# Performance work log

Measured on AMD Instinct MI355X. Metric: run time of the kernel, lower is better.

The kernel has to match this reference:

```python
import jax, jax.numpy as jnp
import numpy as np

B_SZ = 8
G = 2048
D_MODEL = 512
D_STATE = 128
D_CONV = 4
EXPAND = 2
HEADDIM = 64
D_INNER = EXPAND * D_MODEL          # 1024
NHEADS = D_INNER // HEADDIM         # 16
CONV_DIM = D_INNER + 2 * D_STATE    # 1280
D_IN_PROJ = 2 * D_INNER + 2 * D_STATE + NHEADS  # 2320
ID_DIM = 128
CHR_DIM = 64
N_CHR = 25
F_LOCUS = 32
PATH_DIM = 128
GENE_FEAT = ID_DIM + PATH_DIM + 2 * CHR_DIM  # 384
N_PERT = 10000
P_DIM = 128


def silu(x):
    return x * jax.nn.sigmoid(x)


def causal_dw_conv(x, w, b):
    # x: (B,L,C), w: (C,K), b: (C,)  causal depthwise conv (left pad K-1)
    K = w.shape[1]
    L = x.shape[1]
    xp = jnp.pad(x, ((0, 0), (K - 1, 0), (0, 0)))
    out = b[None, None, :]
    for k in range(K):
        out = out + xp[:, k:k + L, :] * w[:, k][None, None, :]
    return out


def mamba2(u, in_w, conv_w, conv_b, dt_bias, A_log, Dp, norm_w, out_w):
    # u: (B,L,d_model) -> (B,L,d_model); mamba_ssm Mamba2 defaults, ngroups=1
    Bb, L, _ = u.shape
    zxbcdt = u @ in_w.T                                   # (B,L,D_IN_PROJ)
    z = zxbcdt[..., :D_INNER]
    xBC = zxbcdt[..., D_INNER:D_INNER + CONV_DIM]
    dt = zxbcdt[..., D_INNER + CONV_DIM:]                 # (B,L,H)
    xBC = silu(causal_dw_conv(xBC, conv_w, conv_b))
    x = xBC[..., :D_INNER].reshape(Bb, L, NHEADS, HEADDIM)
    Bm = xBC[..., D_INNER:D_INNER + D_STATE]              # (B,L,N)
    Cm = xBC[..., D_INNER + D_STATE:]                     # (B,L,N)
    dt = jax.nn.softplus(dt + dt_bias)                    # (B,L,H)
    dA = jnp.exp(dt * (-jnp.exp(A_log)))                  # (B,L,H)

    def step(h, inp):
        dA_t, dt_t, B_t, C_t, x_t = inp
        h = dA_t[:, :, None, None] * h + jnp.einsum('bh,bn,bhp->bhpn', dt_t, B_t, x_t)
        y = jnp.einsum('bhpn,bn->bhp', h, C_t)
        return h, y

    h0 = jnp.zeros((Bb, NHEADS, HEADDIM, D_STATE), u.dtype)
    xs = (dA.transpose(1, 0, 2), dt.transpose(1, 0, 2),
          Bm.transpose(1, 0, 2), Cm.transpose(1, 0, 2), x.transpose(1, 0, 2, 3))
    _, ys = jax.lax.scan(step, h0, xs)                    # ys: (L,B,H,P)
    y = ys.transpose(1, 0, 2, 3) + Dp[None, None, :, None] * x
    y = y.reshape(Bb, L, D_INNER)
    # gated RMSNorm (norm_before_gate=False): norm(y * silu(z))
    y = y * silu(z)
    y = y * jax.lax.rsqrt(jnp.mean(y * y, axis=-1, keepdims=True) + 1e-5) * norm_w
    return y @ out_w.T


def setup_inputs() -> dict:
    key = jax.random.key(0)
    ks = iter(jax.random.split(key, 48))

    def nrm(shape, scale):
        return jax.random.normal(next(ks), shape, jnp.float32) * scale

    inp = {}
    inp['perturbation_idx'] = jax.random.randint(next(ks), (B_SZ,), 0, N_PERT)
    inp['chr_idx'] = jax.random.randint(next(ks), (G,), 0, N_CHR)
    inp['locus_fourier'] = nrm((G, 2 * F_LOCUS), 1.0)
    inp['pathway_features'] = nrm((G, PATH_DIM), 1.0)
    inp['pert_emb'] = nrm((N_PERT, P_DIM), 0.02)
    inp['gene_id_emb'] = nrm((G, ID_DIM), 0.02)
    inp['chr_emb'] = nrm((N_CHR, CHR_DIM), 0.02)
    inp['locus_w'] = nrm((CHR_DIM, 2 * F_LOCUS), (2 * F_LOCUS) ** -0.5)
    inp['locus_b'] = jnp.zeros((CHR_DIM,), jnp.float32)
    inp['cond_w'] = nrm((GENE_FEAT, P_DIM), P_DIM ** -0.5)
    inp['cond_b'] = jnp.zeros((GENE_FEAT,), jnp.float32)
    inp['in_w'] = nrm((D_MODEL, GENE_FEAT), GENE_FEAT ** -0.5)
    inp['in_b'] = jnp.zeros((D_MODEL,), jnp.float32)
    inp['head_w'] = nrm((1, D_MODEL), D_MODEL ** -0.5)
    inp['head_b'] = jnp.zeros((1,), jnp.float32)
    for p in ('f_', 'b_'):
        inp[p + 'in_w'] = nrm((D_IN_PROJ, D_MODEL), D_MODEL ** -0.5)
        inp[p + 'conv_w'] = nrm((CONV_DIM, D_CONV), D_CONV ** -0.5)
        inp[p + 'conv_b'] = jnp.zeros((CONV_DIM,), jnp.float32)
        inp[p + 'dt_bias'] = nrm((NHEADS,), 0.5)
        inp[p + 'A_log'] = jnp.log(jax.random.uniform(next(ks), (NHEADS,), jnp.float32, 1.0, 16.0))
        inp[p + 'D'] = jnp.ones((NHEADS,), jnp.float32)
        inp[p + 'norm_w'] = jnp.ones((D_INNER,), jnp.float32)
        inp[p + 'out_w'] = nrm((D_MODEL, D_INNER), D_INNER ** -0.5)
    return inp


def reference(perturbation_idx, chr_idx, locus_fourier, pathway_features,
              pert_emb, gene_id_emb, chr_emb, locus_w, locus_b,
              cond_w, cond_b, in_w, in_b, head_w, head_b,
              f_in_w, f_conv_w, f_conv_b, f_dt_bias, f_A_log, f_D, f_norm_w, f_out_w,
              b_in_w, b_conv_w, b_conv_b, b_dt_bias, b_A_log, b_D, b_norm_w, b_out_w):
    B = perturbation_idx.shape[0]
    cond = pert_emb[perturbation_idx] @ cond_w.T + cond_b          # (B, GENE_FEAT)
    e_chr = chr_emb[chr_idx]                                        # (G, CHR_DIM)
    e_locus = jax.nn.gelu(locus_fourier @ locus_w.T + locus_b, approximate=False)
    gene_feat = jnp.concatenate([gene_id_emb, pathway_features, e_chr, e_locus], axis=1)  # (G, GENE_FEAT)
    seq = jnp.concatenate([cond[:, None, :],
                           jnp.broadcast_to(gene_feat[None], (B,) + gene_feat.shape)], axis=1)
    seq = seq @ in_w.T + in_b                                       # (B, G+1, d_model)
    h_fwd = mamba2(seq, f_in_w, f_conv_w, f_conv_b, f_dt_bias, f_A_log, f_D, f_norm_w, f_out_w)
    h_bwd = jnp.flip(mamba2(jnp.flip(seq, axis=1), b_in_w, b_conv_w, b_conv_b,
                            b_dt_bias, b_A_log, b_D, b_norm_w, b_out_w), axis=1)
    H = h_fwd + h_bwd
    return H[:, 1:, :] @ head_w.T + head_b                          # (B, G, 1)
```

## Files before the change

### kernel.cpp

```cpp
#include <hip/hip_runtime.h>
#include <hip/hip_bf16.h>
#include <hip/hip_fp16.h>
#include <math.h>

#define DPROJ 2320
#define CONVD 1280

typedef __attribute__((ext_vector_type(8))) short bf16x8;
typedef __attribute__((ext_vector_type(4))) float f32x4;

__device__ __forceinline__ float siluf(float x) { return x / (1.f + __expf(-x)); }
__device__ __forceinline__ float bfu(unsigned short s) { return __uint_as_float(((unsigned)s) << 16); }
__device__ __forceinline__ unsigned short f2bf(float f) {
    unsigned u = __float_as_uint(f);
    unsigned r = (u + 0x7FFFu + ((u >> 16) & 1u)) >> 16;
    return (unsigned short)r;
}
__device__ __forceinline__ unsigned short f2h(float f) {
    __half h = __float2half(f);
    return *(unsigned short*)&h;
}
__device__ __forceinline__ float h2f(unsigned short s) {
    __half h = *(__half*)&s;
    return __half2float(h);
}


__global__ void gg_kernel(const int* __restrict__ chridx, const float* __restrict__ gid,
                          const float* __restrict__ path, const float* __restrict__ chrE,
                          const int* __restrict__ pidx, const float* __restrict__ pertE,
                          float* __restrict__ gf, float* __restrict__ cemb,
                          float* __restrict__ wf2, float* __restrict__ wb2) {
    int blk = blockIdx.x, tid = threadIdx.x;
    if (blk < 3072) {
        int idx = blk * 256 + tid;
        int g = idx / 384, j = idx % 384;
        float v;
        if (j < 128)      v = gid[(size_t)g * 128 + j];
        else if (j < 256) v = path[(size_t)g * 128 + (j - 128)];
        else if (j < 320) v = chrE[(size_t)chridx[g] * 64 + (j - 256)];
        else return;
        gf[idx] = v;
    } else if (blk < 3076) {
        int idx = (blk - 3072) * 256 + tid;
        int b = idx >> 7, k = idx & 127;
        cemb[idx] = pertE[(size_t)pidx[b] * 128 + k];
    } else {
        wf2[tid * 4 + 0] = 0.f; wf2[tid * 4 + 1] = 0.f;
        wf2[tid * 4 + 2] = 0.f; wf2[tid * 4 + 3] = 0.f;
        wb2[tid * 4 + 0] = 0.f; wb2[tid * 4 + 1] = 0.f;
        wb2[tid * 4 + 2] = 0.f; wb2[tid * 4 + 3] = 0.f;
    }
}

__global__ void wfold_kernel(const float* __restrict__ headW,
                             const float* __restrict__ fOutW, const float* __restrict__ fNw,
                             const float* __restrict__ bOutW, const float* __restrict__ bNw,
                             float* __restrict__ wf2, float* __restrict__ wb2) {
    int blk = blockIdx.x;
    int dir = blk >> 6;
    int rem = blk & 63;
    int dseg = rem >> 4, mseg = rem & 15;
    int tid = threadIdx.x;
    int d = dseg * 256 + tid;
    const float* W = dir ? bOutW : fOutW;
    float s = 0.f;
#pragma unroll
    for (int m = mseg * 32; m < mseg * 32 + 32; ++m)
        s += headW[m] * W[(size_t)m * 1024 + d];
    const float* nw = dir ? bNw : fNw;
    atomicAdd(&(dir ? wb2 : wf2)[d], s * nw[d]);
}


__global__ void tobf4_kernel(const float* __restrict__ inW, const float* __restrict__ fInW,
                             const float* __restrict__ bInW, const float* __restrict__ gf,
                             unsigned short* __restrict__ inW2, unsigned short* __restrict__ fInW2,
                             unsigned short* __restrict__ bInW2, unsigned short* __restrict__ gf2) {
    size_t idx = (size_t)blockIdx.x * 256 + threadIdx.x;
    const size_t A = 512UL * 384, B5 = 2432UL * 512;
    if (idx < A) {
        inW2[idx] = f2bf(inW[idx]);
    } else if (idx < A + B5) {
        size_t k = idx - A; int m = k / 512, kk = k % 512;
        fInW2[k] = f2bf(m < 2320 ? fInW[(size_t)m * 512 + kk] : 0.f);
    } else if (idx < A + 2 * B5) {
        size_t k = idx - A - B5; int m = k / 512, kk = k % 512;
        bInW2[k] = f2bf(m < 2320 ? bInW[(size_t)m * 512 + kk] : 0.f);
    } else {
        size_t k = idx - A - 2 * B5;
        gf2[k] = f2bf(gf[k]);
    }
}


__global__ __launch_bounds__(256) void mfma_gemm_kernel(
    const unsigned short* __restrict__ A2, const unsigned short* __restrict__ W2,
    const float* __restrict__ bias, unsigned short* __restrict__ Cbf,
    int N, int K2, int ldc) {
    __shared__ __align__(16) unsigned short Al[128 * 40];
    __shared__ __align__(16) unsigned short Bl[128 * 40];
    const int tid = threadIdx.x;
    const int bm = blockIdx.y * 128, bn = blockIdx.x * 128;
    const int lane = tid & 63, wave = tid >> 6;
    const int wm = (wave >> 1) * 64, wn = (wave & 1) * 64;
    f32x4 acc[4][4];
#pragma unroll
    for (int i = 0; i < 4; ++i)
#pragma unroll
        for (int j = 0; j < 4; ++j) acc[i][j] = (f32x4){0.f, 0.f, 0.f, 0.f};

    for (int k0 = 0; k0 < K2; k0 += 32) {
        __syncthreads();
#pragma unroll
        for (int s = 0; s < 2; ++s) {
            int ch = tid + 256 * s;
            int row = ch >> 2, q = ch & 3;
            uint4 va = *(const uint4*)&A2[(size_t)(bm + row) * K2 + k0 + q * 8];
            *(uint4*)&Al[row * 40 + q * 8] = va;
            uint4 vb = *(const uint4*)&W2[(size_t)(bn + row) * K2 + k0 + q * 8];
            *(uint4*)&Bl[row * 40 + q * 8] = vb;
        }
        __syncthreads();
        bf16x8 af[4], bfr[4];
#pragma unroll
        for (int i = 0; i < 4; ++i)
            af[i] = *(const bf16x8*)&Al[(wm + i * 16 + (lane & 15)) * 40 + (lane >> 4) * 8];
#pragma unroll
        for (int j = 0; j < 4; ++j)
            bfr[j] = *(const bf16x8*)&Bl[(wn + j * 16 + (lane & 15)) * 40 + (lane >> 4) * 8];
#pragma unroll
        for (int i = 0; i < 4; ++i)
#pragma unroll
            for (int j = 0; j < 4; ++j)
                acc[i][j] = __builtin_amdgcn_mfma_f32_16x16x32_bf16(af[i], bfr[j], acc[i][j], 0, 0, 0);
    }
#pragma unroll
    for (int i = 0; i < 4; ++i) {
        int m = bm + wm + i * 16 + (lane >> 4) * 4;
#pragma unroll
        for (int j = 0; j < 4; ++j) {
            int n = bn + wn + j * 16 + (lane & 15);
            if (n < N) {
                float bv = bias ? bias[n] : 0.f;
#pragma unroll
                for (int r = 0; r < 4; ++r)
                    Cbf[(size_t)(m + r) * ldc + n] = f2bf(acc[i][j][r] + bv);
            }
        }
    }
}


__global__ __launch_bounds__(256) void zx_gemm_kernel(
    const unsigned short* __restrict__ A2,
    const unsigned short* __restrict__ fInW2, const unsigned short* __restrict__ bInW2,
    unsigned short* __restrict__ szF, unsigned short* __restrict__ xbcF, float* __restrict__ dtrF,
    unsigned short* __restrict__ szB, unsigned short* __restrict__ xbcB, float* __restrict__ dtrB) {
    __shared__ __align__(16) unsigned short Al[128 * 40];
    __shared__ __align__(16) unsigned short Bl[128 * 40];
    const int tid = threadIdx.x;
    const int bxx = blockIdx.x;
    const int d = (bxx >= 19);
    const int bn = (d ? bxx - 19 : bxx) * 128, bm = blockIdx.y * 128;
    const unsigned short* W2 = d ? bInW2 : fInW2;
    unsigned short* sz = d ? szB : szF;
    unsigned short* xbc = d ? xbcB : xbcF;
    float* dtr = d ? dtrB : dtrF;
    const int lane = tid & 63, wave = tid >> 6;
    const int wm = (wave >> 1) * 64, wn = (wave & 1) * 64;
    const int K2 = 512, N = 2320;
    f32x4 acc[4][4];
#pragma unroll
    for (int i = 0; i < 4; ++i)
#pragma unroll
        for (int j = 0; j < 4; ++j) acc[i][j] = (f32x4){0.f, 0.f, 0.f, 0.f};

    for (int k0 = 0; k0 < K2; k0 += 32) {
        __syncthreads();
#pragma unroll
        for (int s = 0; s < 2; ++s) {
            int ch = tid + 256 * s;
            int row = ch >> 2, q = ch & 3;
            uint4 va = *(const uint4*)&A2[(size_t)(bm + row) * K2 + k0 + q * 8];
            *(uint4*)&Al[row * 40 + q * 8] = va;
            uint4 vb = *(const uint4*)&W2[(size_t)(bn + row) * K2 + k0 + q * 8];
            *(uint4*)&Bl[row * 40 + q * 8] = vb;
        }
        __syncthreads();
        bf16x8 af[4], bfr[4];
#pragma unroll
        for (int i = 0; i < 4; ++i)
            af[i] = *(const bf16x8*)&Al[(wm + i * 16 + (lane & 15)) * 40 + (lane >> 4) * 8];
#pragma unroll
        for (int j = 0; j < 4; ++j)
            bfr[j] = *(const bf16x8*)&Bl[(wn + j * 16 + (lane & 15)) * 40 + (lane >> 4) * 8];
#pragma unroll
        for (int i = 0; i < 4; ++i)
#pragma unroll
            for (int j = 0; j < 4; ++j)
                acc[i][j] = __builtin_amdgcn_mfma_f32_16x16x32_bf16(af[i], bfr[j], acc[i][j], 0, 0, 0);
    }
#pragma unroll
    for (int i = 0; i < 4; ++i) {
        int m = bm + wm + i * 16 + (lane >> 4) * 4;
#pragma unroll
        for (int j = 0; j < 4; ++j) {
            int n = bn + wn + j * 16 + (lane & 15);
            if (n < N) {
#pragma unroll
                for (int r = 0; r < 4; ++r) {
                    float v = acc[i][j][r];
                    if (n < 1024)
                        sz[(size_t)(m + r) * 1024 + n] = f2h(siluf(v));
                    else if (n < 2304)
                        xbc[(size_t)(m + r) * 1280 + (n - 1024)] = f2bf(v);
                    else
                        dtr[(size_t)(m + r) * 16 + (n - 2304)] = v;
                }
            }
        }
    }
}


__global__ __launch_bounds__(256) void gemm_kernel(
    const float* __restrict__ A, const float* __restrict__ W,
    const float* __restrict__ bias, float* __restrict__ C,
    int M, int N, int K, int ldc, int act) {
    __shared__ __align__(16) float As[16][68];
    __shared__ __align__(16) float Ws[16][68];
    const int tid = threadIdx.x;
    const int tx = tid & 15, ty = tid >> 4;
    const int bm = blockIdx.y * 64, bn = blockIdx.x * 64;
    const int lr = tid >> 2;
    const int lk = (tid & 3) * 4;
    float acc[4][4];
#pragma unroll
    for (int i = 0; i < 4; ++i)
#pragma unroll
        for (int j = 0; j < 4; ++j) acc[i][j] = 0.f;

    for (int k0 = 0; k0 < K; k0 += 16) {
        const int am = bm + lr;
        const int wn = bn + lr;
        float4 av = make_float4(0.f, 0.f, 0.f, 0.f), wv = make_float4(0.f, 0.f, 0.f, 0.f);
        if (am < M) av = *(const float4*)&A[(size_t)am * K + k0 + lk];
        if (wn < N) wv = *(const float4*)&W[(size_t)wn * K + k0 + lk];
        __syncthreads();
        As[lk + 0][lr] = av.x; As[lk + 1][lr] = av.y; As[lk + 2][lr] = av.z; As[lk + 3][lr] = av.w;
        Ws[lk + 0][lr] = wv.x; Ws[lk + 1][lr] = wv.y; Ws[lk + 2][lr] = wv.z; Ws[lk + 3][lr] = wv.w;
        __syncthreads();
#pragma unroll
        for (int kk = 0; kk < 16; ++kk) {
            float4 a = *(const float4*)&As[kk][ty * 4];
            float4 w = *(const float4*)&Ws[kk][tx * 4];
            float aa[4] = {a.x, a.y, a.z, a.w}, ww[4] = {w.x, w.y, w.z, w.w};
#pragma unroll
            for (int i = 0; i < 4; ++i)
#pragma unroll
                for (int j = 0; j < 4; ++j) acc[i][j] += aa[i] * ww[j];
        }
    }
#pragma unroll
    for (int i = 0; i < 4; ++i) {
        const int m = bm + ty * 4 + i;
        if (m >= M) continue;
#pragma unroll
        for (int j = 0; j < 4; ++j) {
            const int n = bn + tx * 4 + j;
            if (n >= N) continue;
            float v = acc[i][j] + (bias ? bias[n] : 0.f);
            if (act == 1) v = 0.5f * v * (1.f + erff(v * 0.70710678118654752f));
            C[(size_t)m * ldc + n] = v;
        }
    }
}


__global__ void dt_kernel(const float* __restrict__ dtrF, const float* __restrict__ dtrB,
                          const float* __restrict__ zxc,
                          const float* __restrict__ fDtB, const float* __restrict__ bDtB,
                          float* __restrict__ dtFsT, float* __restrict__ dtBsT,
                          float* __restrict__ dtFp) {
    int idx = blockIdx.x * 256 + threadIdx.x;
    if (idx < 32768) {
        int r = idx >> 4, hh = idx & 15;
        float raw = dtrF[idx] + fDtB[hh];
        dtFsT[hh * 2048 + r] = (raw > 20.f) ? raw : log1pf(expf(raw));
    } else if (idx < 65536) {
        int k = idx - 32768;
        int r = k >> 4, hh = k & 15;
        float raw = dtrB[(size_t)(2047 - r) * 16 + hh] + bDtB[hh];
        dtBsT[hh * 2048 + r] = (raw > 20.f) ? raw : log1pf(expf(raw));
    } else if (idx < 65664) {
        int k = idx - 65536;
        int b = k >> 4, hh = k & 15;
        float raw = zxc[(size_t)b * DPROJ + 2304 + hh] + fDtB[hh];
        dtFp[k] = (raw > 20.f) ? raw : log1pf(expf(raw));
    }
}

__global__ void cum_kernel(const float* __restrict__ dtFsT, const float* __restrict__ dtBsT,
                           const float* __restrict__ fAlog, const float* __restrict__ bAlog,
                           float* __restrict__ cumF, float* __restrict__ cumB) {
    int id = blockIdx.x * 256 + threadIdx.x;
    int dir = id >> 9, k = id & 511, h = k >> 5, c = k & 31;
    const float* dtT = dir ? dtBsT : dtFsT;
    const float* Al = dir ? bAlog : fAlog;
    float* cum = dir ? cumB : cumF;
    float a = -expf(Al[h]);
    float acc = 0.f;
    for (int s4 = 0; s4 < 16; ++s4) {
        float4 v = *(const float4*)&dtT[h * 2048 + c * 64 + s4 * 4];
        float4 o;
        acc += v.x * a; o.x = acc;
        acc += v.y * a; o.y = acc;
        acc += v.z * a; o.z = acc;
        acc += v.w * a; o.w = acc;
        *(float4*)&cum[h * 2048 + c * 64 + s4 * 4] = o;
    }
}


__global__ void conv_kernel(const unsigned short* __restrict__ xbcF,
                            const unsigned short* __restrict__ xbcB,
                            const float* __restrict__ zxc,
                            const float* __restrict__ fCw, const float* __restrict__ fCb,
                            const float* __restrict__ bCw, const float* __restrict__ bCb,
                            unsigned short* __restrict__ bcF, unsigned short* __restrict__ xF16,
                            unsigned short* __restrict__ bcB, unsigned short* __restrict__ xB16,
                            float* __restrict__ convFp, unsigned short* __restrict__ bcFp,
                            unsigned short* __restrict__ xFp16) {
    int blk = blockIdx.x, tid = threadIdx.x;
    if (blk < 10225) {
        int idx = blk * 256 + tid;
        if (idx >= 2045 * 1280) return;
        int t4 = idx / 1280, c = idx % 1280;
        float4 w4 = *(const float4*)&fCw[c * 4];
        float acc = fCb[c];
        acc += bfu(xbcF[(size_t)(t4 + 0) * 1280 + c]) * w4.x;
        acc += bfu(xbcF[(size_t)(t4 + 1) * 1280 + c]) * w4.y;
        acc += bfu(xbcF[(size_t)(t4 + 2) * 1280 + c]) * w4.z;
        acc += bfu(xbcF[(size_t)(t4 + 3) * 1280 + c]) * w4.w;
        float r = siluf(acc);
        if (c >= 1024) bcF[(size_t)t4 * 256 + (c - 1024)] = f2bf(r);
        else           xF16[(size_t)t4 * 1024 + c] = f2bf(r);
    } else if (blk < 20465) {
        int idx = (blk - 10225) * 256 + tid;
        int s = idx / 1280, c = idx % 1280;
        float4 w4 = *(const float4*)&bCw[c * 4];
        float w[4] = {w4.x, w4.y, w4.z, w4.w};
        float acc = bCb[c];
#pragma unroll
        for (int k = 0; k < 4; ++k) {
            int j = s - 3 + k;
            if (j >= 0) acc += bfu(xbcB[(size_t)(2047 - j) * 1280 + c]) * w[k];
        }
        float r = siluf(acc);
        if (c >= 1024) bcB[(size_t)s * 256 + (c - 1024)] = f2bf(r);
        else           xB16[(size_t)s * 1024 + c] = f2bf(r);
    } else {
        int idx = (blk - 20465) * 256 + tid;
        int b = idx / 5120;
        int r = idx % 5120;
        int t = r / 1280, c = r % 1280;
        float4 w4 = *(const float4*)&fCw[c * 4];
        float w[4] = {w4.x, w4.y, w4.z, w4.w};
        float acc = fCb[c];
#pragma unroll
        for (int k = 0; k < 4; ++k) {
            int j = t - 3 + k;
            float x = 0.f;
            if (j == 0)      x = zxc[(size_t)b * DPROJ + 1024 + c];
            else if (j >= 1) x = bfu(xbcF[(size_t)(j - 1) * 1280 + c]);
            acc += x * w[k];
        }
        float rr = siluf(acc);
        convFp[idx] = rr;
        if (c >= 1024) bcFp[(size_t)(b * 4 + t) * 256 + (c - 1024)] = f2bf(rr);
        else           xFp16[(size_t)(b * 4 + t) * 1024 + c] = f2bf(rr);
    }
}


__global__ __launch_bounds__(256) void intra_kernel(
    const unsigned short* __restrict__ bcF, const unsigned short* __restrict__ bcFp,
    const unsigned short* __restrict__ bcB,
    const unsigned short* __restrict__ xF16, const unsigned short* __restrict__ xFp16,
    const unsigned short* __restrict__ xB16,
    const float* __restrict__ dtFsT, const float* __restrict__ dtBsT,
    const float* __restrict__ cumF, const float* __restrict__ cumB,
    unsigned short* __restrict__ YiF0, unsigned short* __restrict__ YiFs,
    unsigned short* __restrict__ YiB,
    unsigned short* __restrict__ UF0, unsigned short* __restrict__ UFs,
    unsigned short* __restrict__ UB) {
    __shared__ __align__(16) unsigned char smraw[63232];
    unsigned short* Bt = (unsigned short*)smraw;
    unsigned short* Ct = (unsigned short*)(smraw + 17408);
    unsigned short* Sm = (unsigned short*)(smraw + 17408);
    unsigned short* BT = (unsigned short*)(smraw + 34816);
    unsigned short* XT = (unsigned short*)(smraw + 53248);
    float* scum = (float*)(smraw + 62464);
    float* sdt  = scum + 64;
    float* se   = scum + 128;

    const int iid = blockIdx.x;
    int dir, b = 0, h, c;
    unsigned short *Yout, *Uout;
    if (iid < 128)      { dir = 0; b = iid >> 4; h = iid & 15; c = 0;
                          Yout = YiF0 + (size_t)(b * 16 + h) * 4096; Uout = UF0 + (size_t)(b * 16 + h) * 8192; }
    else if (iid < 624) { int k = iid - 128; dir = 0; c = 1 + (k >> 4); h = k & 15;
                          Yout = YiFs + (size_t)(c * 16 + h) * 4096; Uout = UFs + (size_t)(c * 16 + h) * 8192; }
    else                { int k = iid - 624; dir = 1; c = k >> 4; h = k & 15;
                          Yout = YiB + (size_t)(c * 16 + h) * 4096;  Uout = UB + (size_t)(c * 16 + h) * 8192; }
    const float* dtAT = dir ? dtBsT : dtFsT;
    const float* cumA = dir ? cumB : cumF;

    const int tid = threadIdx.x;
    const int lane = tid & 63, wave = tid >> 6;
    const int quad = lane >> 4, l15 = lane & 15;

    {
        int r = tid >> 2, q = tid & 3;
        const unsigned short *bsrc, *xsrc;
        if (dir == 0) {
            int t = 64 * c + 1 + r;
            if (t < 4) { bsrc = bcFp + (size_t)(b * 4 + t) * 256; xsrc = xFp16 + (size_t)(b * 4 + t) * 1024; }
            else       { bsrc = bcF + (size_t)(t - 4) * 256;      xsrc = xF16 + (size_t)(t - 4) * 1024; }
        } else {
            int s = 64 * c + r;
            bsrc = bcB + (size_t)s * 256;
            xsrc = xB16 + (size_t)s * 1024;
        }
#pragma unroll
        for (int i = 0; i < 4; ++i) {
            int n0 = q * 32 + i * 8;
            uint4 v = *(const uint4*)&bsrc[n0];
            *(uint4*)&Bt[r * 136 + n0] = v;
            const unsigned short* pv = (const unsigned short*)&v;
#pragma unroll
            for (int jj = 0; jj < 8; ++jj) BT[(n0 + jj) * 72 + r] = pv[jj];
        }
#pragma unroll
        for (int i = 0; i < 4; ++i) {
            int n0 = q * 32 + i * 8;
            uint4 v = *(const uint4*)&bsrc[128 + n0];
            *(uint4*)&Ct[r * 136 + n0] = v;
        }
#pragma unroll
        for (int k = 0; k < 2; ++k) {
            uint4 v = *(const uint4*)&xsrc[h * 64 + q * 16 + k * 8];
            const unsigned short* pv = (const unsigned short*)&v;
#pragma unroll
            for (int jj = 0; jj < 8; ++jj) XT[(q * 16 + k * 8 + jj) * 72 + r] = pv[jj];
        }
        if (tid < 64) {
            int j = 64 * c + tid;
            scum[tid] = cumA[h * 2048 + j];
            sdt[tid] = dtAT[h * 2048 + j];
        }
    }
    __syncthreads();
    if (tid < 64) se[tid] = __expf(scum[63] - scum[tid]) * sdt[tid];

    const int tm = (wave >> 1) * 32, sn = (wave & 1) * 32;
    f32x4 acc1[2][2];
#pragma unroll
    for (int i = 0; i < 2; ++i)
#pragma unroll
        for (int j = 0; j < 2; ++j) acc1[i][j] = (f32x4){0.f, 0.f, 0.f, 0.f};
#pragma unroll
    for (int ks = 0; ks < 4; ++ks) {
        bf16x8 af[2], bfr[2];
#pragma unroll
        for (int i = 0; i < 2; ++i)
            af[i] = *(const bf16x8*)&Ct[(tm + i * 16 + l15) * 136 + ks * 32 + quad * 8];
#pragma unroll
        for (int j = 0; j < 2; ++j)
            bfr[j] = *(const bf16x8*)&Bt[(sn + j * 16 + l15) * 136 + ks * 32 + quad * 8];
#pragma unroll
        for (int i = 0; i < 2; ++i)
#pragma unroll
            for (int j = 0; j < 2; ++j)
                acc1[i][j] = __builtin_amdgcn_mfma_f32_16x16x32_bf16(af[i], bfr[j], acc1[i][j], 0, 0, 0);
    }
    __syncthreads();

#pragma unroll
    for (int j = 0; j < 2; ++j) {
        int s = sn + j * 16 + l15;
        float cs = scum[s], ds = sdt[s];
#pragma unroll
        for (int i = 0; i < 2; ++i) {
#pragma unroll
            for (int r = 0; r < 4; ++r) {
                int t = tm + i * 16 + quad * 4 + r;
                float v = (s <= t) ? __expf(scum[t] - cs) * ds * acc1[i][j][r] : 0.f;
                Sm[t * 72 + s] = f2bf(v);
            }
        }
    }
    __syncthreads();

    const int pm = (wave >> 1) * 32, tn = (wave & 1) * 32;
    f32x4 acc2[2][2];
#pragma unroll
    for (int i = 0; i < 2; ++i)
#pragma unroll
        for (int j = 0; j < 2; ++j) acc2[i][j] = (f32x4){0.f, 0.f, 0.f, 0.f};
#pragma unroll
    for (int ks = 0; ks < 2; ++ks) {
        bf16x8 af[2], bfr[2];
#pragma unroll
        for (int i = 0; i < 2; ++i)
            af[i] = *(const bf16x8*)&XT[(pm + i * 16 + l15) * 72 + ks * 32 + quad * 8];
#pragma unroll
        for (int j = 0; j < 2; ++j)
            bfr[j] = *(const bf16x8*)&Sm[(tn + j * 16 + l15) * 72 + ks * 32 + quad * 8];
#pragma unroll
        for (int i = 0; i < 2; ++i)
#pragma unroll
            for (int j = 0; j < 2; ++j)
                acc2[i][j] = __builtin_amdgcn_mfma_f32_16x16x32_bf16(af[i], bfr[j], acc2[i][j], 0, 0, 0);
    }
#pragma unroll
    for (int i = 0; i < 2; ++i)
#pragma unroll
        for (int j = 0; j < 2; ++j) {
            int t = tn + j * 16 + l15;
            int p0 = pm + i * 16 + quad * 4;
            ushort4 o = make_ushort4(f2bf(acc2[i][j][0]), f2bf(acc2[i][j][1]),
                                     f2bf(acc2[i][j][2]), f2bf(acc2[i][j][3]));
            *(ushort4*)&Yout[t * 64 + p0] = o;
        }

    const int nm = wave * 32;
    f32x4 acc3[2][4];
#pragma unroll
    for (int i = 0; i < 2; ++i)
#pragma unroll
        for (int j = 0; j < 4; ++j) acc3[i][j] = (f32x4){0.f, 0.f, 0.f, 0.f};
#pragma unroll
    for (int ks = 0; ks < 2; ++ks) {
        float ev[8];
#pragma unroll
        for (int jj = 0; jj < 8; ++jj) ev[jj] = se[ks * 32 + quad * 8 + jj];
        bf16x8 bfx[4];
#pragma unroll
        for (int j = 0; j < 4; ++j) {
            bf16x8 xs = *(const bf16x8*)&XT[(j * 16 + l15) * 72 + ks * 32 + quad * 8];
#pragma unroll
            for (int jj = 0; jj < 8; ++jj)
                bfx[j][jj] = (short)f2bf(bfu((unsigned short)xs[jj]) * ev[jj]);
        }
        bf16x8 af[2];
#pragma unroll
        for (int i = 0; i < 2; ++i)
            af[i] = *(const bf16x8*)&BT[(nm + i * 16 + l15) * 72 + ks * 32 + quad * 8];
#pragma unroll
        for (int i = 0; i < 2; ++i)
#pragma unroll
            for (int j = 0; j < 4; ++j)
                acc3[i][j] = __builtin_amdgcn_mfma_f32_16x16x32_bf16(af[i], bfx[j], acc3[i][j], 0, 0, 0);
    }
#pragma unroll
    for (int i = 0; i < 2; ++i)
#pragma unroll
        for (int j = 0; j < 4; ++j) {
            int p = j * 16 + l15;
            int n0 = nm + i * 16 + quad * 4;
            ushort4 o = make_ushort4(f2bf(acc3[i][j][0]), f2bf(acc3[i][j][1]),
                                     f2bf(acc3[i][j][2]), f2bf(acc3[i][j][3]));
            *(ushort4*)&Uout[p * 128 + n0] = o;
        }
}


__global__ void mid_kernel(const float* __restrict__ convFp, const unsigned short* __restrict__ bcF,
                           const float* __restrict__ dtFp, const float* __restrict__ cumF,
                           const float* __restrict__ cumB,
                           const unsigned short* __restrict__ UF0,
                           const unsigned short* __restrict__ UFs, const unsigned short* __restrict__ UB,
                           float* __restrict__ cb0, unsigned short* __restrict__ Mb,
                           unsigned short* __restrict__ Tst, float* __restrict__ psiF) {
    int blk = blockIdx.x, tid = threadIdx.x;
    if (blk < 32) {
        int idx = blk * 256 + tid;
        int b = idx >> 10, r = idx & 1023, h = r >> 6, tl = r & 63;
        int t = tl + 1;
        const float* b0 = convFp + (size_t)(b * 4) * CONVD;
        float s = 0.f;
        if (t < 4) {
            const float* crow = convFp + (size_t)(b * 4 + t) * CONVD;
            for (int n = 0; n < 128; ++n) s += crow[1152 + n] * b0[1024 + n];
        } else {
            const unsigned short* cr = bcF + (size_t)(t - 4) * 256 + 128;
            for (int n = 0; n < 128; ++n) s += bfu(cr[n]) * b0[1024 + n];
        }
        cb0[(b * 16 + h) * 64 + tl] = s * dtFp[b * 16 + h];
    } else if (blk < 160) {
        int bh = blk - 32;
        int b = bh >> 4, h = bh & 15;
        float D0 = __expf(cumF[h * 2048 + 63]);
        float dt0 = dtFp[b * 16 + h];
        const float* row0 = convFp + (size_t)(b * 4) * CONVD;
        const unsigned short* u = UF0 + (size_t)(b * 16 + h) * 8192;
        unsigned short* m = Mb + (size_t)(b * 16 + h) * 8192;
        for (int e4 = tid; e4 < 2048; e4 += 256) {
            int e = e4 * 4, p = e >> 7, n0 = e & 127;
            float s = D0 * dt0 * row0[h * 64 + p];
            float4 B4 = *(const float4*)&row0[1024 + n0];
            ushort4 uv = *(const ushort4*)&u[e];
            ushort4 o = make_ushort4(f2bf(s * B4.x + bfu(uv.x)), f2bf(s * B4.y + bfu(uv.y)),
                                     f2bf(s * B4.z + bfu(uv.z)), f2bf(s * B4.w + bfu(uv.w)));
            *(ushort4*)&m[e] = o;
        }
    } else {
        int blk2 = blk - 160;
        int dir = blk2 >> 7, h = (blk2 >> 3) & 15, q8 = blk2 & 7;
        const unsigned short* U = dir ? UB : UFs;
        const float* cum = dir ? cumB : cumF;
        unsigned short* T = Tst + (size_t)(dir * 16 + h) * 32 * 8192;
        if (dir == 0 && q8 == 0 && tid == 0) {
            float ps = 1.f;
            for (int c = 1; c < 32; ++c) {
                psiF[h * 32 + c] = ps;
                ps *= __expf(cumF[h * 2048 + c * 64 + 63]);
            }
        }
        const size_t e = (size_t)q8 * 1024 + 4 * tid;
        float4 st = make_float4(0.f, 0.f, 0.f, 0.f);
        const int c0 = dir ? 0 : 1;
        ushort4 u = *(const ushort4*)&U[((size_t)c0 * 16 + h) * 8192 + e];
        for (int c = c0; c < 32; ++c) {
            ushort4 un = make_ushort4(0, 0, 0, 0);
            if (c + 1 < 32) un = *(const ushort4*)&U[((size_t)(c + 1) * 16 + h) * 8192 + e];
            float Dc = __expf(cum[h * 2048 + c * 64 + 63]);
            ushort4 o = make_ushort4(f2bf(st.x), f2bf(st.y), f2bf(st.z), f2bf(st.w));
            *(ushort4*)&T[(size_t)c * 8192 + e] = o;
            st.x = Dc * st.x + bfu(u.x);
            st.y = Dc * st.y + bfu(u.y);
            st.z = Dc * st.z + bfu(u.z);
            st.w = Dc * st.w + bfu(u.w);
            u = un;
        }
    }
}


__global__ __launch_bounds__(256) void yt_kernel(
    const unsigned short* __restrict__ bcF, const unsigned short* __restrict__ bcB,
    const unsigned short* __restrict__ Tst,
    const unsigned short* __restrict__ YiFs, const unsigned short* __restrict__ YiB,
    const unsigned short* __restrict__ xF16, const unsigned short* __restrict__ xB16,
    const float* __restrict__ cumF, const float* __restrict__ cumB,
    const float* __restrict__ fD, const float* __restrict__ bD,
    unsigned short* __restrict__ YsF, unsigned short* __restrict__ YsB) {
    const int iid = blockIdx.x;
    int dir, h, c;
    if (iid < 496) { dir = 0; c = 1 + (iid >> 4); h = iid & 15; }
    else           { int k = iid - 496; dir = 1; c = k >> 4; h = k & 15; }
    const unsigned short* Cbase = (dir == 0)
        ? bcF + ((size_t)(64 * c - 3)) * 256 + 128
        : bcB + ((size_t)(64 * c)) * 256 + 128;
    const unsigned short* Tp = Tst + ((size_t)(dir * 16 + h) * 32 + c) * 8192;
    const unsigned short* Yi = (dir == 0 ? YiFs : YiB) + (size_t)(c * 16 + h) * 4096;
    const unsigned short* xbase = (dir == 0) ? xF16 + ((size_t)(64 * c - 3)) * 1024
                                             : xB16 + ((size_t)(64 * c)) * 1024;
    const float* cum = dir ? cumB : cumF;
    const float Dh = (dir ? bD : fD)[h];
    unsigned short* Ys = (dir == 0 ? YsF : YsB) + (size_t)(c * 16 + h) * 4096;
    const int tid = threadIdx.x;
    const int lane = tid & 63, wave = tid >> 6;
    const int quad = lane >> 4, l15 = lane & 15;
    const int pm = (wave >> 1) * 32, tb = (wave & 1) * 32;
    f32x4 acc[2][2];
#pragma unroll
    for (int i = 0; i < 2; ++i)
#pragma unroll
        for (int j = 0; j < 2; ++j) acc[i][j] = (f32x4){0.f, 0.f, 0.f, 0.f};
#pragma unroll
    for (int ks = 0; ks < 4; ++ks) {
        bf16x8 af[2], bfr[2];
#pragma unroll
        for (int i = 0; i < 2; ++i)
            af[i] = *(const bf16x8*)&Tp[(size_t)(pm + i * 16 + l15) * 128 + ks * 32 + quad * 8];
#pragma unroll
        for (int j = 0; j < 2; ++j)
            bfr[j] = *(const bf16x8*)&Cbase[(size_t)(tb + j * 16 + l15) * 256 + ks * 32 + quad * 8];
#pragma unroll
        for (int i = 0; i < 2; ++i)
#pragma unroll
            for (int j = 0; j < 2; ++j)
                acc[i][j] = __builtin_amdgcn_mfma_f32_16x16x32_bf16(af[i], bfr[j], acc[i][j], 0, 0, 0);
    }
#pragma unroll
    for (int i = 0; i < 2; ++i)
#pragma unroll
        for (int j = 0; j < 2; ++j) {
            int t = tb + j * 16 + l15;
            int p0 = pm + i * 16 + quad * 4;
            float et = __expf(cum[h * 2048 + 64 * c + t]);
            ushort4 yi = *(const ushort4*)&Yi[t * 64 + p0];
            ushort4 xv = *(const ushort4*)&xbase[(size_t)t * 1024 + h * 64 + p0];
            ushort4 o = make_ushort4(f2bf(bfu(yi.x) + et * acc[i][j][0] + Dh * bfu(xv.x)),
                                     f2bf(bfu(yi.y) + et * acc[i][j][1] + Dh * bfu(xv.y)),
                                     f2bf(bfu(yi.z) + et * acc[i][j][2] + Dh * bfu(xv.z)),
                                     f2bf(bfu(yi.w) + et * acc[i][j][3] + Dh * bfu(xv.w)));
            *(ushort4*)&Ys[t * 64 + p0] = o;
        }
}


__global__ __launch_bounds__(256) void gate_kernel(
    const unsigned short* __restrict__ bcF,
    const unsigned short* __restrict__ Mb, const float* __restrict__ psiF,
    const unsigned short* __restrict__ YsF, const unsigned short* __restrict__ YsB,
    const unsigned short* __restrict__ xF16, const unsigned short* __restrict__ xFp16,
    const unsigned short* __restrict__ szF, const unsigned short* __restrict__ szB,
    const float* __restrict__ convFp,
    const float* __restrict__ cumF,
    const unsigned short* __restrict__ YiF0,
    const float* __restrict__ cb0,
    const float* __restrict__ fD,
    const float* __restrict__ wf2, const float* __restrict__ wb2,
    float* __restrict__ aF, float* __restrict__ aB) {
    __shared__ __align__(16) float Ysm[64 * 68];

    const int iid = blockIdx.x;
    int dir, b = 0, h, cg;
    if (iid < 2048) { dir = 0; b = iid >> 8; int r = iid & 255; h = r >> 4; cg = r & 15; }
    else            { int k = iid - 2048; dir = 1; h = k >> 4; cg = k & 15; }
    const int tid = threadIdx.x, tx = tid & 15, ty = tid >> 4;
    const int lane = tid & 63, wave = tid >> 6;
    const int quad = lane >> 4, l15 = lane & 15;

    const float Dh = dir ? 0.f : fD[h];
    const float* wvp = dir ? wb2 : wf2;
    float4 wreg = *(const float4*)&wvp[h * 64 + tx * 4];

    const int pm = (wave >> 1) * 32, tb = (wave & 1) * 32;
    bf16x8 mfr[4][2];
    if (dir == 0) {
        const unsigned short* Mp = Mb + (size_t)(b * 16 + h) * 8192;
#pragma unroll
        for (int ks = 0; ks < 4; ++ks)
#pragma unroll
            for (int i = 0; i < 2; ++i)
                mfr[ks][i] = *(const bf16x8*)&Mp[(size_t)(pm + i * 16 + l15) * 128 + ks * 32 + quad * 8];
    }

    for (int cc = 0; cc < 2; ++cc) {
        const int c = cg * 2 + cc;
        const bool fwdG = (dir == 0 && c > 0);
        const bool c0 = (dir == 0 && c == 0);

        float rawet[4];
        ushort4 y4a[4], z4a[4], x4a[4];
#pragma unroll
        for (int i = 0; i < 4; ++i) {
            int tl = ty + 16 * i;
            int j = 64 * c + tl;
            rawet[i] = (dir == 0) ? cumF[h * 2048 + j] : 0.f;
            const unsigned short *Yp, *zp;
            if (dir == 0) {
                Yp = c0 ? YiF0 + (size_t)(b * 16 + h) * 4096 : YsF + (size_t)(c * 16 + h) * 4096;
                zp = szF + (size_t)j * 1024;
            } else {
                Yp = YsB + (size_t)(c * 16 + h) * 4096;
                zp = szB + (size_t)(2047 - j) * 1024;
            }
            y4a[i] = *(const ushort4*)&Yp[tl * 64 + tx * 4];
            z4a[i] = *(const ushort4*)&zp[h * 64 + tx * 4];
            if (c0) {
                int t = j + 1;
                const unsigned short* xp = (t < 4) ? xFp16 + (size_t)(b * 4 + t) * 1024
                                                   : xF16 + (size_t)(t - 4) * 1024;
                x4a[i] = *(const ushort4*)&xp[h * 64 + tx * 4];
            } else {
                x4a[i] = make_ushort4(0, 0, 0, 0);
            }
        }
        float4 x0v = make_float4(0.f, 0.f, 0.f, 0.f);
        float cbv[4] = {0.f, 0.f, 0.f, 0.f};
        if (c0) {
            x0v = *(const float4*)&convFp[(size_t)(b * 4) * CONVD + h * 64 + tx * 4];
#pragma unroll
            for (int i = 0; i < 4; ++i) cbv[i] = cb0[(b * 16 + h) * 64 + (ty + 16 * i)];
        }

        if (fwdG) {
            if (cc > 0) __syncthreads();
            const unsigned short* Cbase = bcF + ((size_t)(64 * c - 3)) * 256 + 128;
            f32x4 acc[2][2];
#pragma unroll
            for (int i = 0; i < 2; ++i)
#pragma unroll
                for (int j = 0; j < 2; ++j) acc[i][j] = (f32x4){0.f, 0.f, 0.f, 0.f};
#pragma unroll
            for (int ks = 0; ks < 4; ++ks) {
                bf16x8 bfr[2];
#pragma unroll
                for (int j = 0; j < 2; ++j)
                    bfr[j] = *(const bf16x8*)&Cbase[(size_t)(tb + j * 16 + l15) * 256 + ks * 32 + quad * 8];
#pragma unroll
                for (int i = 0; i < 2; ++i)
#pragma unroll
                    for (int j = 0; j < 2; ++j)
                        acc[i][j] = __builtin_amdgcn_mfma_f32_16x16x32_bf16(mfr[ks][i], bfr[j], acc[i][j], 0, 0, 0);
            }
#pragma unroll
            for (int i = 0; i < 2; ++i)
#pragma unroll
                for (int j = 0; j < 2; ++j)
                    *(f32x4*)&Ysm[(tb + j * 16 + l15) * 68 + pm + i * 16 + quad * 4] = acc[i][j];
            __syncthreads();
        }

        const float psi = fwdG ? psiF[h * 32 + c] : 0.f;

#pragma unroll
        for (int i = 0; i < 4; ++i) {
            int tl = ty + 16 * i;
            int j = 64 * c + tl;
            float k1 = 0.f;
            float cma[4] = {0.f, 0.f, 0.f, 0.f};
            if (fwdG) {
                float et = __expf(rawet[i]);
                k1 = et * psi;
                float4 cmv = *(const float4*)&Ysm[tl * 68 + tx * 4];
                cma[0] = cmv.x; cma[1] = cmv.y; cma[2] = cmv.z; cma[3] = cmv.w;
            } else if (c0) {
                float et = __expf(rawet[i]);
                k1 = et * cbv[i];
                cma[0] = x0v.x; cma[1] = x0v.y; cma[2] = x0v.z; cma[3] = x0v.w;
            }
            float yv[4] = {bfu(y4a[i].x), bfu(y4a[i].y), bfu(y4a[i].z), bfu(y4a[i].w)};
            float sza[4] = {h2f(z4a[i].x), h2f(z4a[i].y), h2f(z4a[i].z), h2f(z4a[i].w)};
            float xa[4] = {bfu(x4a[i].x), bfu(x4a[i].y), bfu(x4a[i].z), bfu(x4a[i].w)};
            float wa[4] = {wreg.x, wreg.y, wreg.z, wreg.w};
            float a1 = 0.f, a2 = 0.f;
#pragma unroll
            for (int w = 0; w < 4; ++w) {
                float tot = yv[w] + k1 * cma[w] + (c0 ? Dh * xa[w] : 0.f);
                float g = tot * sza[w];
                a1 += g * wa[w];
                a2 += g * g;
            }
#pragma unroll
            for (int m = 1; m < 16; m <<= 1) {
                a1 += __shfl_xor(a1, m);
                a2 += __shfl_xor(a2, m);
            }
            if (tx == 0) {
                if (dir == 0) {
                    size_t o = ((size_t)(b * 2048 + j) * 16 + h) * 2;
                    aF[o] = a1; aF[o + 1] = a2;
                } else {
                    int g = 2047 - j;
                    size_t o = ((size_t)g * 16 + h) * 2;
                    aB[o] = a1; aB[o + 1] = a2;
                }
            }
        }
    }
}


__global__ void final_kernel(const float* __restrict__ aF, const float* __restrict__ aB,
                             const float* __restrict__ headB, float* __restrict__ out) {
    int idx = blockIdx.x * 256 + threadIdx.x;
    int b = idx >> 11, g = idx & 2047;
    const float* pf = aF + ((size_t)(b * 2048 + g)) * 32;
    const float* pb = aB + (size_t)g * 32;
    float f1 = 0.f, f2 = 0.f, b1 = 0.f, b2 = 0.f;
#pragma unroll
    for (int h = 0; h < 16; ++h) {
        f1 += pf[2 * h]; f2 += pf[2 * h + 1];
        b1 += pb[2 * h]; b2 += pb[2 * h + 1];
    }
    out[idx] = f1 * rsqrtf(f2 * (1.f / 1024.f) + 1e-5f) +
               b1 * rsqrtf(b2 * (1.f / 1024.f) + 1e-5f) + headB[0];
}


extern "C" void kernel_launch(void* const* d_in, const int* in_sizes, int n_in,
                              void* d_out, int out_size, void* d_ws, size_t ws_size,
                              hipStream_t stream) {
    const int*   pidx   = (const int*)  d_in[0];
    const int*   chridx = (const int*)  d_in[1];
    const float* locusF = (const float*)d_in[2];
    const float* pathF  = (const float*)d_in[3];
    const float* pertE  = (const float*)d_in[4];
    const float* gidE   = (const float*)d_in[5];
    const float* chrE   = (const float*)d_in[6];
    const float* locusW = (const float*)d_in[7];
    const float* locusB = (const float*)d_in[8];
    const float* condW  = (const float*)d_in[9];
    const float* condB  = (const float*)d_in[10];
    const float* inW    = (const float*)d_in[11];
    const float* inB    = (const float*)d_in[12];
    const float* headW  = (const float*)d_in[13];
    const float* headB  = (const float*)d_in[14];
    const float* fInW   = (const float*)d_in[15];
    const float* fCw    = (const float*)d_in[16];
    const float* fCb    = (const float*)d_in[17];
    const float* fDtB   = (const float*)d_in[18];
    const float* fAlog  = (const float*)d_in[19];
    const float* fDp    = (const float*)d_in[20];
    const float* fNw    = (const float*)d_in[21];
    const float* fOutW  = (const float*)d_in[22];
    const float* bInW   = (const float*)d_in[23];
    const float* bCw    = (const float*)d_in[24];
    const float* bCb    = (const float*)d_in[25];
    const float* bDtB   = (const float*)d_in[26];
    const float* bAlog  = (const float*)d_in[27];
    const float* bDp    = (const float*)d_in[28];
    const float* bNw    = (const float*)d_in[29];
    const float* bOutW  = (const float*)d_in[30];
    float* out = (float*)d_out;
    (void)in_sizes; (void)n_in; (void)out_size; (void)ws_size;

    char* base = (char*)d_ws;
    size_t off = 0;
    auto allocf = [&](size_t n) -> float* {
        char* r = base + off; off += ((n * 4 + 63) & ~(size_t)63); return (float*)r; };
    auto allocu = [&](size_t n) -> unsigned short* {
        char* r = base + off; off += ((n * 2 + 63) & ~(size_t)63); return (unsigned short*)r; };

    float* gf     = allocf(2048UL * 384);
    float* cond   = allocf(8UL * 384);
    float* cemb   = allocf(8UL * 128);
    float* uc     = allocf(8UL * 512);
    float* zxc    = allocf(8UL * DPROJ);
    float* convFp = allocf(8UL * 4 * CONVD);
    float* dtrF   = allocf(2048UL * 16);
    float* dtrB   = allocf(2048UL * 16);
    float* dtFsT  = allocf(16UL * 2048);
    float* dtFp   = allocf(128);
    float* dtBsT  = allocf(16UL * 2048);
    float* cumF   = allocf(16UL * 2048);
    float* cumB   = allocf(16UL * 2048);
    float* wf2    = allocf(1024);
    float* wb2    = allocf(1024);
    float* cb0    = allocf(8UL * 16 * 64);
    float* psiF   = allocf(16UL * 32);
    float* aF     = allocf(8UL * 2048 * 16 * 2);
    float* aB     = allocf(2048UL * 16 * 2);
    unsigned short* xbcF = allocu(2048UL * 1280);
    unsigned short* xbcB = allocu(2048UL * 1280);
    unsigned short* YiF0 = allocu(8UL * 16 * 4096);
    unsigned short* YiFs = allocu(32UL * 16 * 4096);
    unsigned short* YiB  = allocu(32UL * 16 * 4096);
    unsigned short* UF0  = allocu(8UL * 16 * 8192);
    unsigned short* UFs  = allocu(32UL * 16 * 8192);
    unsigned short* UB   = allocu(32UL * 16 * 8192);
    unsigned short* Mb   = allocu(8UL * 16 * 8192);
    unsigned short* Tst  = allocu(2UL * 16 * 32 * 8192);
    unsigned short* bcF  = allocu(2045UL * 256);
    unsigned short* bcFp = allocu(32UL * 256);
    unsigned short* bcB  = allocu(2048UL * 256);
    unsigned short* YsF  = allocu(32UL * 16 * 4096);
    unsigned short* YsB  = allocu(32UL * 16 * 4096);
    unsigned short* xF16 = allocu(2045UL * 1024);
    unsigned short* xFp16= allocu(32UL * 1024);
    unsigned short* xB16 = allocu(2048UL * 1024);
    unsigned short* szF  = allocu(2048UL * 1024);
    unsigned short* szB  = allocu(2048UL * 1024);
    unsigned short* gf2   = allocu(2048UL * 384);
    unsigned short* inW2  = allocu(512UL * 384);
    unsigned short* ug2   = allocu(2048UL * 512);
    unsigned short* fInW2 = allocu(2432UL * 512);
    unsigned short* bInW2 = allocu(2432UL * 512);

    gg_kernel<<<3077, 256, 0, stream>>>(chridx, gidE, pathF, chrE, pidx, pertE, gf, cemb, wf2, wb2);
    wfold_kernel<<<128, 256, 0, stream>>>(headW, fOutW, fNw, bOutW, bNw, wf2, wb2);
    gemm_kernel<<<dim3(1, 32), 256, 0, stream>>>(locusF, locusW, locusB, gf + 320, 2048, 64, 64, 384, 1);
    gemm_kernel<<<dim3(6, 1), 256, 0, stream>>>(cemb, condW, condB, cond, 8, 384, 128, 384, 0);

    tobf4_kernel<<<13568, 256, 0, stream>>>(inW, fInW, bInW, gf, inW2, fInW2, bInW2, gf2);

    mfma_gemm_kernel<<<dim3(4, 16), 256, 0, stream>>>(gf2, inW2, inB, ug2, 512, 384, 512);
    gemm_kernel<<<dim3(8, 1), 256, 0, stream>>>(cond, inW, inB, uc, 8, 512, 384, 512, 0);

    zx_gemm_kernel<<<dim3(38, 16), 256, 0, stream>>>(ug2, fInW2, bInW2,
                                                     szF, xbcF, dtrF, szB, xbcB, dtrB);
    gemm_kernel<<<dim3(37, 1), 256, 0, stream>>>(uc, fInW, nullptr, zxc, 8, DPROJ, 512, DPROJ, 0);

    dt_kernel<<<257, 256, 0, stream>>>(dtrF, dtrB, zxc, fDtB, bDtB, dtFsT, dtBsT, dtFp);
    cum_kernel<<<4, 256, 0, stream>>>(dtFsT, dtBsT, fAlog, bAlog, cumF, cumB);
    conv_kernel<<<20625, 256, 0, stream>>>(xbcF, xbcB, zxc, fCw, fCb, bCw, bCb,
                                           bcF, xF16, bcB, xB16, convFp, bcFp, xFp16);
    intra_kernel<<<1136, 256, 0, stream>>>(bcF, bcFp, bcB, xF16, xFp16, xB16,
                                           dtFsT, dtBsT, cumF, cumB,
                                           YiF0, YiFs, YiB, UF0, UFs, UB);
    mid_kernel<<<416, 256, 0, stream>>>(convFp, bcF, dtFp, cumF, cumB, UF0, UFs, UB,
                                        cb0, Mb, Tst, psiF);
    yt_kernel<<<1008, 256, 0, stream>>>(bcF, bcB, Tst, YiFs, YiB, xF16, xB16,
                                        cumF, cumB, fDp, bDp, YsF, YsB);
    gate_kernel<<<2304, 256, 0, stream>>>(bcF, Mb, psiF, YsF, YsB, xF16, xFp16,
                                          szF, szB, convFp, cumF,
                                          YiF0, cb0, fDp, wf2, wb2, aF, aB);
    final_kernel<<<64, 256, 0, stream>>>(aF, aB, headB, out);
}
```

Baseline: 366.4 us.

## Fuse small prologue GEMMs and dt/cumsum kernels, alias intra_kernel shared buffers

Folds the locus GELU projection and the conditioning projection into gg_kernel as naive per-thread dot products, removing two gemm_kernel launches. It also merges dt_kernel into cum_kernel so softplus and the cumulative sum are computed in one pass, removing another launch. In intra_kernel, the transposed B tile now shares shared memory with Bt and is written after the first phase, which shrinks LDS use to allow more resident blocks. The trade-offs are a cum_kernel that does serial strided loads and transcendentals on only 5 blocks, and extra register pressure from holding the B vectors.

Measured after the change: 401.0 us. 1.09x slower.

```diff
diff --git a/kernel.cpp b/kernel.cpp
--- a/kernel.cpp
+++ b/kernel.cpp
@@ -29,7 +29,10 @@
 __global__ void gg_kernel(const int* __restrict__ chridx, const float* __restrict__ gid,
                           const float* __restrict__ path, const float* __restrict__ chrE,
                           const int* __restrict__ pidx, const float* __restrict__ pertE,
-                          float* __restrict__ gf, float* __restrict__ cemb,
+                          const float* __restrict__ locusF, const float* __restrict__ locusW,
+                          const float* __restrict__ locusB,
+                          const float* __restrict__ condW, const float* __restrict__ condB,
+                          float* __restrict__ gf, float* __restrict__ cond,
                           float* __restrict__ wf2, float* __restrict__ wb2) {
     int blk = blockIdx.x, tid = threadIdx.x;
     if (blk < 3072) {
@@ -41,15 +44,29 @@
         else if (j < 320) v = chrE[(size_t)chridx[g] * 64 + (j - 256)];
         else return;
         gf[idx] = v;
-    } else if (blk < 3076) {
-        int idx = (blk - 3072) * 256 + tid;
-        int b = idx >> 7, k = idx & 127;
-        cemb[idx] = pertE[(size_t)pidx[b] * 128 + k];
-    } else {
+    } else if (blk == 3072) {
         wf2[tid * 4 + 0] = 0.f; wf2[tid * 4 + 1] = 0.f;
         wf2[tid * 4 + 2] = 0.f; wf2[tid * 4 + 3] = 0.f;
         wb2[tid * 4 + 0] = 0.f; wb2[tid * 4 + 1] = 0.f;
         wb2[tid * 4 + 2] = 0.f; wb2[tid * 4 + 3] = 0.f;
+    } else if (blk < 3585) {
+        int idx = (blk - 3073) * 256 + tid;
+        int g = idx >> 6, d = idx & 63;
+        float acc = locusB[d];
+#pragma unroll 8
+        for (int k = 0; k < 64; ++k)
+            acc += locusF[(size_t)g * 64 + k] * locusW[(size_t)d * 64 + k];
+        float v = 0.5f * acc * (1.f + erff(acc * 0.70710678118654752f));
+        gf[(size_t)g * 384 + 320 + d] = v;
+    } else {
+        int idx = (blk - 3585) * 256 + tid;
+        int r = idx / 384, n = idx % 384;
+        const float* pe = pertE + (size_t)pidx[r] * 128;
+        float acc = condB[n];
+#pragma unroll 8
+        for (int k = 0; k < 128; ++k)
+            acc += pe[k] * condW[(size_t)n * 128 + k];
+        cond[(size_t)r * 384 + n] = acc;
     }
 }
 
@@ -278,47 +295,36 @@
 }
 
 
-__global__ void dt_kernel(const float* __restrict__ dtrF, const float* __restrict__ dtrB,
-                          const float* __restrict__ zxc,
-                          const float* __restrict__ fDtB, const float* __restrict__ bDtB,
-                          float* __restrict__ dtFsT, float* __restrict__ dtBsT,
-                          float* __restrict__ dtFp) {
-    int idx = blockIdx.x * 256 + threadIdx.x;
-    if (idx < 32768) {
-        int r = idx >> 4, hh = idx & 15;
-        float raw = dtrF[idx] + fDtB[hh];
-        dtFsT[hh * 2048 + r] = (raw > 20.f) ? raw : log1pf(expf(raw));
-    } else if (idx < 65536) {
-        int k = idx - 32768;
-        int r = k >> 4, hh = k & 15;
-        float raw = dtrB[(size_t)(2047 - r) * 16 + hh] + bDtB[hh];
-        dtBsT[hh * 2048 + r] = (raw > 20.f) ? raw : log1pf(expf(raw));
-    } else if (idx < 65664) {
-        int k = idx - 65536;
-        int b = k >> 4, hh = k & 15;
-        float raw = zxc[(size_t)b * DPROJ + 2304 + hh] + fDtB[hh];
-        dtFp[k] = (raw > 20.f) ? raw : log1pf(expf(raw));
-    }
-}
-
-__global__ void cum_kernel(const float* __restrict__ dtFsT, const float* __restrict__ dtBsT,
+__global__ void cum_kernel(const float* __restrict__ dtrF, const float* __restrict__ dtrB,
+                           const float* __restrict__ zxc,
+                           const float* __restrict__ fDtB, const float* __restrict__ bDtB,
                            const float* __restrict__ fAlog, const float* __restrict__ bAlog,
+                           float* __restrict__ dtFsT, float* __restrict__ dtBsT,
+                           float* __restrict__ dtFp,
                            float* __restrict__ cumF, float* __restrict__ cumB) {
-    int id = blockIdx.x * 256 + threadIdx.x;
+    int blk = blockIdx.x, tid = threadIdx.x;
+    if (blk == 4) {
+        if (tid < 128) {
+            int b = tid >> 4, hh = tid & 15;
+            float raw = zxc[(size_t)b * DPROJ + 2304 + hh] + fDtB[hh];
+            dtFp[tid] = (raw > 20.f) ? raw : log1pf(expf(raw));
+        }
+        return;
+    }
+    int id = blk * 256 + tid;
     int dir = id >> 9, k = id & 511, h = k >> 5, c = k & 31;
-    const float* dtT = dir ? dtBsT : dtFsT;
-    const float* Al = dir ? bAlog : fAlog;
+    float bias = (dir ? bDtB : fDtB)[h];
+    float a = -expf((dir ? bAlog : fAlog)[h]);
+    float* dtT = dir ? dtBsT : dtFsT;
     float* cum = dir ? cumB : cumF;
-    float a = -expf(Al[h]);
     float acc = 0.f;
-    for (int s4 = 0; s4 < 16; ++s4) {
-        float4 v = *(const float4*)&dtT[h * 2048 + c * 64 + s4 * 4];
-        float4 o;
-        acc += v.x * a; o.x = acc;
-        acc += v.y * a; o.y = acc;
-        acc += v.z * a; o.z = acc;
-        acc += v.w * a; o.w = acc;
-        *(float4*)&cum[h * 2048 + c * 64 + s4 * 4] = o;
+    for (int s = 0; s < 64; ++s) {
+        int j = c * 64 + s;
+        float raw = (dir ? dtrB[(size_t)(2047 - j) * 16 + h] : dtrF[(size_t)j * 16 + h]) + bias;
+        float dt = (raw > 20.f) ? raw : log1pf(expf(raw));
+        dtT[h * 2048 + j] = dt;
+        acc += dt * a;
+        cum[h * 2048 + j] = acc;
     }
 }
 
@@ -395,13 +401,13 @@
     unsigned short* __restrict__ YiB,
     unsigned short* __restrict__ UF0, unsigned short* __restrict__ UFs,
     unsigned short* __restrict__ UB) {
-    __shared__ __align__(16) unsigned char smraw[63232];
+    __shared__ __align__(16) unsigned char smraw[45824];
     unsigned short* Bt = (unsigned short*)smraw;
-    unsigned short* Ct = (unsigned short*)(smraw + 17408);
-    unsigned short* Sm = (unsigned short*)(smraw + 17408);
-    unsigned short* BT = (unsigned short*)(smraw + 34816);
-    unsigned short* XT = (unsigned short*)(smraw + 53248);
-    float* scum = (float*)(smraw + 62464);
+    unsigned short* BT = (unsigned short*)smraw;
+    unsigned short* Ct = (unsigned short*)(smraw + 18432);
+    unsigned short* Sm = (unsigned short*)(smraw + 18432);
+    unsigned short* XT = (unsigned short*)(smraw + 35840);
+    float* scum = (float*)(smraw + 45056);
     float* sdt  = scum + 64;
     float* se   = scum + 128;
 
@@ -420,9 +426,10 @@
     const int tid = threadIdx.x;
     const int lane = tid & 63, wave = tid >> 6;
     const int quad = lane >> 4, l15 = lane & 15;
-
+    const int r = tid >> 2, q = tid & 3;
+
+    uint4 bv[4];
     {
-        int r = tid >> 2, q = tid & 3;
         const unsigned short *bsrc, *xsrc;
         if (dir == 0) {
             int t = 64 * c + 1 + r;
@@ -436,11 +443,8 @@
 #pragma unroll
         for (int i = 0; i < 4; ++i) {
             int n0 = q * 32 + i * 8;
-            uint4 v = *(const uint4*)&bsrc[n0];
-            *(uint4*)&Bt[r * 136 + n0] = v;
-            const unsigned short* pv = (const unsigned short*)&v;
-#pragma unroll
-            for (int jj = 0; jj < 8; ++jj) BT[(n0 + jj) * 72 + r] = pv[jj];
+            bv[i] = *(const uint4*)&bsrc[n0];
+            *(uint4*)&Bt[r * 136 + n0] = bv[i];
         }
 #pragma unroll
         for (int i = 0; i < 4; ++i) {
@@ -494,12 +498,19 @@
 #pragma unroll
         for (int i = 0; i < 2; ++i) {
 #pragma unroll
-            for (int r = 0; r < 4; ++r) {
-                int t = tm + i * 16 + quad * 4 + r;
-                float v = (s <= t) ? __expf(scum[t] - cs) * ds * acc1[i][j][r] : 0.f;
+            for (int rr = 0; rr < 4; ++rr) {
+                int t = tm + i * 16 + quad * 4 + rr;
+                float v = (s <= t) ? __expf(scum[t] - cs) * ds * acc1[i][j][rr] : 0.f;
                 Sm[t * 72 + s] = f2bf(v);
             }
         }
+    }
+#pragma unroll
+    for (int i = 0; i < 4; ++i) {
+        int n0 = q * 32 + i * 8;
+        const unsigned short* pv = (const unsigned short*)&bv[i];
+#pragma unroll
+        for (int jj = 0; jj < 8; ++jj) BT[(n0 + jj) * 72 + r] = pv[jj];
     }
     __syncthreads();
 
@@ -931,7 +942,6 @@
 
     float* gf     = allocf(2048UL * 384);
     float* cond   = allocf(8UL * 384);
-    float* cemb   = allocf(8UL * 128);
     float* uc     = allocf(8UL * 512);
     float* zxc    = allocf(8UL * DPROJ);
     float* convFp = allocf(8UL * 4 * CONVD);
@@ -974,11 +984,10 @@
     unsigned short* fInW2 = allocu(2432UL * 512);
     unsigned short* bInW2 = allocu(2432UL * 512);
 
-    gg_kernel<<<3077, 256, 0, stream>>>(chridx, gidE, pathF, chrE, pidx, pertE, gf, cemb, wf2, wb2);
+    gg_kernel<<<3597, 256, 0, stream>>>(chridx, gidE, pathF, chrE, pidx, pertE,
+                                        locusF, locusW, locusB, condW, condB,
+                                        gf, cond, wf2, wb2);
     wfold_kernel<<<128, 256, 0, stream>>>(headW, fOutW, fNw, bOutW, bNw, wf2, wb2);
-    gemm_kernel<<<dim3(1, 32), 256, 0, stream>>>(locusF, locusW, locusB, gf + 320, 2048, 64, 64, 384, 1);
-    gemm_kernel<<<dim3(6, 1), 256, 0, stream>>>(cemb, condW, condB, cond, 8, 384, 128, 384, 0);
-
     tobf4_kernel<<<13568, 256, 0, stream>>>(inW, fInW, bInW, gf, inW2, fInW2, bInW2, gf2);
 
     mfma_gemm_kernel<<<dim3(4, 16), 256, 0, stream>>>(gf2, inW2, inB, ug2, 512, 384, 512);
@@ -988,8 +997,8 @@
                                                      szF, xbcF, dtrF, szB, xbcB, dtrB);
     gemm_kernel<<<dim3(37, 1), 256, 0, stream>>>(uc, fInW, nullptr, zxc, 8, DPROJ, 512, DPROJ, 0);
 
-    dt_kernel<<<257, 256, 0, stream>>>(dtrF, dtrB, zxc, fDtB, bDtB, dtFsT, dtBsT, dtFp);
-    cum_kernel<<<4, 256, 0, stream>>>(dtFsT, dtBsT, fAlog, bAlog, cumF, cumB);
+    cum_kernel<<<5, 256, 0, stream>>>(dtrF, dtrB, zxc, fDtB, bDtB, fAlog, bAlog,
+                                      dtFsT, dtBsT, dtFp, cumF, cumB);
     conv_kernel<<<20625, 256, 0, stream>>>(xbcF, xbcB, zxc, fCw, fCb, bCw, bCb,
                                            bcF, xF16, bcB, xB16, convFp, bcFp, xFp16);
     intra_kernel<<<1136, 256, 0, stream>>>(bcF, bcFp, bcB, xF16, xFp16, xB16,
```
